# Performance work log

Hardware: AMD Instinct MI355X
Metric: run time of the kernel (lower is better)

The kernel has to match this reference:

```python
import jax, jax.numpy as jnp
import numpy as np
import math

B, S, H, NH = 2, 2048, 2048, 16
HD = H // NH
BASE = 10000.0


def _rope_tables():
    inv_freq = 1.0 / (BASE ** (np.arange(0, HD, 2, dtype=np.float32) / HD))
    t = np.arange(S, dtype=np.float32)
    freqs = np.einsum('i,j->ij', t, inv_freq)          # [S, HD/2]
    emb = np.concatenate([freqs, freqs], axis=-1)       # [S, HD]
    return jnp.asarray(np.cos(emb)), jnp.asarray(np.sin(emb))


def setup_inputs() -> dict:
    key = jax.random.key(0)
    ks = jax.random.split(key, 6)
    scale = 1.0 / math.sqrt(H)
    cos, sin = _rope_tables()
    causal = np.triu(np.full((S, S), -1e9, dtype=np.float32), k=1)
    attn_bias = jnp.broadcast_to(jnp.asarray(causal)[None, None], (B, 1, S, S))
    return {
        'hidden_states': jax.random.normal(ks[0], (B, S, H), jnp.float32),
        'masks': jnp.zeros((B, S, S), jnp.float32),
        'attn_bias': attn_bias,
        'cos': cos,
        'sin': sin,
        'wq': jax.random.normal(ks[1], (H, H), jnp.float32) * scale,
        'wk': jax.random.normal(ks[2], (H, H), jnp.float32) * scale,
        'wv': jax.random.normal(ks[3], (H, H), jnp.float32) * scale,
        'wo': jax.random.normal(ks[4], (H, H), jnp.float32) * scale,
        'position_ids': jnp.broadcast_to(jnp.arange(S, dtype=jnp.int64)[None], (B, S)),
    }


def _rotate_half(x):
    x1, x2 = x[..., : x.shape[-1] // 2], x[..., x.shape[-1] // 2:]
    return jnp.concatenate([-x2, x1], axis=-1)


def reference(hidden_states, masks, attn_bias, cos, sin, wq, wk, wv, wo, position_ids):
    b, s, h = hidden_states.shape
    nh, hd = NH, HD
    # QKV projections (torch Linear: x @ W.T), split heads -> [b, nh, s, hd]
    def proj(w):
        return (hidden_states @ w.T).reshape(b, s, nh, hd).transpose(0, 2, 1, 3)
    q, k, v = proj(wq), proj(wk), proj(wv)
    # RoPE
    cos_p = cos[position_ids][:, None]  # [b, 1, s, hd]
    sin_p = sin[position_ids][:, None]
    q = q * cos_p + _rotate_half(q) * sin_p
    k = k * cos_p + _rotate_half(k) * sin_p
    # attention scores with additive masks (mx_attn branch, fp math)
    att = jnp.einsum('bhqd,bhkd->bhqk', q / math.sqrt(hd), k)
    att = att + attn_bias + masks[:, None]
    att = jax.nn.softmax(att, axis=-1)
    out = jnp.einsum('bhqk,bhkd->bhqd', att, v)
    out = out.transpose(0, 2, 1, 3).reshape(b, s, h)
    return out @ wo.T
```

## Files before the change

### kernel.cpp

```cpp
#include <hip/hip_runtime.h>
#include <stdint.h>

#define B_  2
#define S_  2048
#define H_  2048
#define NH_ 16
#define HD_ 128

typedef __bf16 v8bf __attribute__((ext_vector_type(8)));
typedef float  v4f  __attribute__((ext_vector_type(4)));

__device__ __forceinline__ float b2f(unsigned short u) {
  union { unsigned int i; float f; } x; x.i = ((unsigned int)u) << 16; return x.f;
}
__device__ __forceinline__ unsigned short f2b(float f) {
  union { float f; unsigned int i; } x; x.f = f;
  unsigned int r = x.i + 0x7FFFu + ((x.i >> 16) & 1u);
  return (unsigned short)(r >> 16);
}

__device__ __forceinline__ void async16(const void* g, void* l) {
  __builtin_amdgcn_global_load_lds(
      (const __attribute__((address_space(1))) void*)g,
      (__attribute__((address_space(3))) void*)l, 16, 0, 0);
}

__global__ __launch_bounds__(256) void cvt_f32_bf16(const float* __restrict__ src,
                                                    unsigned short* __restrict__ dst,
                                                    int n4) {
  int i = blockIdx.x * 256 + threadIdx.x;
  if (i < n4) {
    float4 f = *(const float4*)(src + (size_t)i * 4);
    ushort4 u;
    u.x = f2b(f.x); u.y = f2b(f.y); u.z = f2b(f.z); u.w = f2b(f.w);
    *(ushort4*)(dst + (size_t)i * 4) = u;
  }
}

__device__ __forceinline__ void gemm_tile_nt(const unsigned short* __restrict__ A,
                                             const unsigned short* __restrict__ Bm,
                                             int m0, int n0, int Kdim,
                                             unsigned short* As, unsigned short* Bs,
                                             v4f (&acc)[4][4]) {
  const int tid = threadIdx.x;
  const int lane = tid & 63, w = tid >> 6;
  const int lr = lane & 15, lg = lane >> 4;
  const int wm = (w >> 1) * 64, wn = (w & 1) * 64;

  for (int k0 = 0; k0 < Kdim; k0 += 32) {
    __syncthreads();
#pragma unroll
    for (int i = 0; i < 2; ++i) {
      const int cbase = i * 256 + w * 64;
      const int cc = cbase + lane;
      const int row = cc >> 2, col = (cc & 3) << 3;
      async16(A  + (size_t)(m0 + row) * Kdim + k0 + col, (char*)As + (size_t)cbase * 16);
      async16(Bm + (size_t)(n0 + row) * Kdim + k0 + col, (char*)Bs + (size_t)cbase * 16);
    }
    __syncthreads();
    v8bf a[4], bb[4];
#pragma unroll
    for (int i = 0; i < 4; i++) a[i]  = *(const v8bf*)(As + (wm + i * 16 + lr) * 32 + lg * 8);
#pragma unroll
    for (int i = 0; i < 4; i++) bb[i] = *(const v8bf*)(Bs + (wn + i * 16 + lr) * 32 + lg * 8);
#pragma unroll
    for (int mi = 0; mi < 4; mi++)
#pragma unroll
      for (int ni = 0; ni < 4; ni++)
        acc[mi][ni] = __builtin_amdgcn_mfma_f32_16x16x32_bf16(a[mi], bb[ni], acc[mi][ni], 0, 0, 0);
  }
}

__global__ __launch_bounds__(256, 2) void gemm_qkv(const unsigned short* __restrict__ X,
                                                   const unsigned short* __restrict__ Wq,
                                                   const unsigned short* __restrict__ Wk,
                                                   const unsigned short* __restrict__ Wv,
                                                   unsigned short* __restrict__ Qo,
                                                   unsigned short* __restrict__ Ko,
                                                   unsigned short* __restrict__ Vo) {
  __shared__ unsigned short As[128 * 32], Bs[128 * 32];
  const int m0 = blockIdx.x * 128;
  const int ny = blockIdx.y;
  const int sel = ny >> 4;
  const unsigned short* Bm = (sel == 0) ? Wq : (sel == 1 ? Wk : Wv);
  unsigned short* Out = (sel == 0) ? Qo : (sel == 1 ? Ko : Vo);
  const int n0 = (ny & 15) * 128;

  v4f acc[4][4];
#pragma unroll
  for (int i = 0; i < 4; i++)
#pragma unroll
    for (int j = 0; j < 4; j++) { v4f z = {0.f, 0.f, 0.f, 0.f}; acc[i][j] = z; }

  gemm_tile_nt(X, Bm, m0, n0, H_, As, Bs, acc);

  const int lane = threadIdx.x & 63, w = threadIdx.x >> 6;
  const int lr = lane & 15, lg = lane >> 4;
  const int wm = (w >> 1) * 64, wn = (w & 1) * 64;
#pragma unroll
  for (int mi = 0; mi < 4; mi++)
#pragma unroll
    for (int ni = 0; ni < 4; ni++)
#pragma unroll
      for (int r = 0; r < 4; r++)
        Out[(size_t)(m0 + wm + mi * 16 + lg * 4 + r) * H_ + n0 + wn + ni * 16 + lr] =
            f2b(acc[mi][ni][r]);
}

__global__ __launch_bounds__(256, 2) void gemm_out(const unsigned short* __restrict__ A,
                                                   const unsigned short* __restrict__ Wo,
                                                   float* __restrict__ Out) {
  __shared__ unsigned short As[128 * 32], Bs[128 * 32];
  const int m0 = blockIdx.x * 128;
  const int n0 = blockIdx.y * 128;

  v4f acc[4][4];
#pragma unroll
  for (int i = 0; i < 4; i++)
#pragma unroll
    for (int j = 0; j < 4; j++) { v4f z = {0.f, 0.f, 0.f, 0.f}; acc[i][j] = z; }

  gemm_tile_nt(A, Wo, m0, n0, H_, As, Bs, acc);

  const int lane = threadIdx.x & 63, w = threadIdx.x >> 6;
  const int lr = lane & 15, lg = lane >> 4;
  const int wm = (w >> 1) * 64, wn = (w & 1) * 64;
#pragma unroll
  for (int mi = 0; mi < 4; mi++)
#pragma unroll
    for (int ni = 0; ni < 4; ni++)
#pragma unroll
      for (int r = 0; r < 4; r++)
        Out[(size_t)(m0 + wm + mi * 16 + lg * 4 + r) * H_ + n0 + wn + ni * 16 + lr] =
            acc[mi][ni][r];
}

__global__ __launch_bounds__(256) void rope_kernel(unsigned short* __restrict__ Q,
                                                   unsigned short* __restrict__ K,
                                                   const float* __restrict__ cosT,
                                                   const float* __restrict__ sinT) {
  unsigned idx = blockIdx.x * 256 + threadIdx.x;
  int dq = (idx & 15) * 4;
  int h  = (idx >> 4) & 15;
  int s  = (idx >> 8) & 2047;
  int b  = idx >> 19;
  size_t base = ((size_t)(b * S_ + s)) * H_ + h * HD_;
  const float* cr = cosT + (size_t)s * HD_;
  const float* sr = sinT + (size_t)s * HD_;
  float c1[4], c2[4], s1[4], s2[4];
#pragma unroll
  for (int j = 0; j < 4; j++) {
    c1[j] = cr[dq + j]; c2[j] = cr[64 + dq + j];
    s1[j] = sr[dq + j]; s2[j] = sr[64 + dq + j];
  }
#pragma unroll
  for (int a = 0; a < 2; a++) {
    unsigned short* P = a == 0 ? Q : K;
    const float sc = (a == 0) ? 0.088388347648318447f : 1.0f;
    ushort4 u1 = *(ushort4*)(P + base + dq);
    ushort4 u2 = *(ushort4*)(P + base + 64 + dq);
    float x1[4] = {b2f(u1.x), b2f(u1.y), b2f(u1.z), b2f(u1.w)};
    float x2[4] = {b2f(u2.x), b2f(u2.y), b2f(u2.z), b2f(u2.w)};
    ushort4 o1, o2;
    o1.x = f2b((x1[0] * c1[0] - x2[0] * s1[0]) * sc);
    o1.y = f2b((x1[1] * c1[1] - x2[1] * s1[1]) * sc);
    o1.z = f2b((x1[2] * c1[2] - x2[2] * s1[2]) * sc);
    o1.w = f2b((x1[3] * c1[3] - x2[3] * s1[3]) * sc);
    o2.x = f2b((x2[0] * c2[0] + x1[0] * s2[0]) * sc);
    o2.y = f2b((x2[1] * c2[1] + x1[1] * s2[1]) * sc);
    o2.z = f2b((x2[2] * c2[2] + x1[2] * s2[2]) * sc);
    o2.w = f2b((x2[3] * c2[3] + x1[3] * s2[3]) * sc);
    *(ushort4*)(P + base + dq) = o1;
    *(ushort4*)(P + base + 64 + dq) = o2;
  }
}

__global__ __launch_bounds__(256) void transpose_v(const unsigned short* __restrict__ Vb,
                                                   unsigned short* __restrict__ Vt) {
  __shared__ unsigned short tile[64][130];
  const int tid = threadIdx.x;
  const int s0 = blockIdx.x * 64;
  const int h = blockIdx.y, b = blockIdx.z;
  for (int i = tid; i < 64 * 64; i += 256) {
    int s = i >> 6, dp = i & 63;
    *(ushort2*)&tile[s][dp * 2] =
        *(const ushort2*)(Vb + (size_t)(b * S_ + s0 + s) * H_ + h * HD_ + dp * 2);
  }
  __syncthreads();
  for (int i = tid; i < 128 * 64; i += 256) {
    int d = i >> 6, s = i & 63;
    Vt[((size_t)((b * NH_ + h) * HD_) + d) * S_ + s0 + s] = tile[s][d];
  }
}

#define KT_ 64

__global__ __launch_bounds__(256, 2) void attn_kernel(const unsigned short* __restrict__ Qb,
                                                      const unsigned short* __restrict__ Kb,
                                                      const unsigned short* __restrict__ Vt,
                                                      unsigned short* __restrict__ Ob) {
  __shared__ __align__(16) char smem[54272];
  unsigned short* Ks = (unsigned short*)smem;
  unsigned short* Vs = (unsigned short*)(smem + 17408);
  unsigned short* Ps = (unsigned short*)(smem + 35840);

  const int tid = threadIdx.x, lane = tid & 63, w = tid >> 6;
  const int lr = lane & 15, lg = lane >> 4;
  const int qt = blockIdx.x, h = blockIdx.y, b = blockIdx.z;
  const int q0 = qt * 128;
  const int wrow = q0 + w * 32;

  v8bf qf[2][4];
#pragma unroll
  for (int mt = 0; mt < 2; mt++)
#pragma unroll
    for (int ks = 0; ks < 4; ks++)
      qf[mt][ks] = *(const v8bf*)(Qb + (size_t)(b * S_ + wrow + mt * 16 + lr) * H_ +
                                  h * HD_ + ks * 32 + lg * 8);

  v4f o[2][8];
#pragma unroll
  for (int mt = 0; mt < 2; mt++)
#pragma unroll
    for (int nt = 0; nt < 8; nt++) { v4f z = {0.f, 0.f, 0.f, 0.f}; o[mt][nt] = z; }
  float mst[2][4], lst[2][4];
#pragma unroll
  for (int mt = 0; mt < 2; mt++)
#pragma unroll
    for (int r = 0; r < 4; r++) { mst[mt][r] = -1e30f; lst[mt][r] = 0.f; }

  const int nkt = (q0 + 128) / KT_;
  for (int kt = 0; kt < nkt; kt++) {
    const int k0 = kt * KT_;
    __syncthreads();
    for (int i = 0; i < 5; ++i) {
      int cbase = i * 256 + w * 64;
      if (cbase < 1088) {
        int cc = cbase + lane;
        int row = cc / 17, pos = cc % 17;
        int p2 = (pos == 16) ? 0 : pos;
        async16(Kb + (size_t)(b * S_ + k0 + row) * H_ + h * HD_ + p2 * 8,
                (char*)Ks + (size_t)cbase * 16);
      }
    }
    for (int i = 0; i < 5; ++i) {
      int cbase = i * 256 + w * 64;
      if (cbase < 1152) {
        int cc = cbase + lane;
        int row = cc / 9, pos = cc % 9;
        int p2 = (pos == 8) ? 0 : pos;
        async16(Vt + ((size_t)((b * NH_ + h) * HD_ + row)) * S_ + k0 + p2 * 8,
                (char*)Vs + (size_t)cbase * 16);
      }
    }
    __syncthreads();

    if (k0 <= wrow + 31) {
      v4f sacc[2][4];
#pragma unroll
      for (int mt = 0; mt < 2; mt++)
#pragma unroll
        for (int nt = 0; nt < 4; nt++) { v4f z = {0.f, 0.f, 0.f, 0.f}; sacc[mt][nt] = z; }
#pragma unroll
      for (int nt = 0; nt < 4; nt++) {
        v8bf kf[4];
#pragma unroll
        for (int ks = 0; ks < 4; ks++)
          kf[ks] = *(const v8bf*)(Ks + (nt * 16 + lr) * 136 + ks * 32 + lg * 8);
#pragma unroll
        for (int mt = 0; mt < 2; mt++)
#pragma unroll
          for (int ks = 0; ks < 4; ks++)
            sacc[mt][nt] =
                __builtin_amdgcn_mfma_f32_16x16x32_bf16(qf[mt][ks], kf[ks], sacc[mt][nt], 0, 0, 0);
      }
      if (k0 + KT_ - 1 > wrow) {
#pragma unroll
        for (int mt = 0; mt < 2; mt++)
#pragma unroll
          for (int nt = 0; nt < 4; nt++)
#pragma unroll
            for (int r = 0; r < 4; r++) {
              int key = k0 + nt * 16 + lr;
              int query = wrow + mt * 16 + lg * 4 + r;
              if (key > query) sacc[mt][nt][r] = -1e30f;
            }
      }
#pragma unroll
      for (int mt = 0; mt < 2; mt++) {
        float rmax[4], alpha[4], rsum[4];
#pragma unroll
        for (int r = 0; r < 4; r++) {
          float v = fmaxf(fmaxf(sacc[mt][0][r], sacc[mt][1][r]),
                          fmaxf(sacc[mt][2][r], sacc[mt][3][r]));
#pragma unroll
          for (int off = 8; off >= 1; off >>= 1) v = fmaxf(v, __shfl_xor(v, off, 64));
          rmax[r] = v;
        }
#pragma unroll
        for (int r = 0; r < 4; r++) {
          float mnew = fmaxf(mst[mt][r], rmax[r]);
          alpha[r] = __expf(mst[mt][r] - mnew);
          mst[mt][r] = mnew;
          rsum[r] = 0.f;
        }
#pragma unroll
        for (int nt = 0; nt < 4; nt++)
#pragma unroll
          for (int r = 0; r < 4; r++) {
            float p = __expf(sacc[mt][nt][r] - mst[mt][r]);
            rsum[r] += p;
            Ps[w * 2304 + (mt * 16 + lg * 4 + r) * 72 + nt * 16 + lr] = f2b(p);
          }
#pragma unroll
        for (int r = 0; r < 4; r++) {
#pragma unroll
          for (int off = 8; off >= 1; off >>= 1) rsum[r] += __shfl_xor(rsum[r], off, 64);
          lst[mt][r] = lst[mt][r] * alpha[r] + rsum[r];
        }
#pragma unroll
        for (int nt = 0; nt < 8; nt++)
#pragma unroll
          for (int r = 0; r < 4; r++) o[mt][nt][r] *= alpha[r];
      }
      asm volatile("" ::: "memory");
      v8bf af[2][2];
#pragma unroll
      for (int mt = 0; mt < 2; mt++)
#pragma unroll
        for (int ks = 0; ks < 2; ks++)
          af[mt][ks] = *(const v8bf*)(Ps + w * 2304 + (mt * 16 + lr) * 72 + ks * 32 + lg * 8);
#pragma unroll
      for (int nt = 0; nt < 8; nt++) {
        v8bf bv[2];
#pragma unroll
        for (int ks = 0; ks < 2; ks++)
          bv[ks] = *(const v8bf*)(Vs + (nt * 16 + lr) * 72 + ks * 32 + lg * 8);
#pragma unroll
        for (int mt = 0; mt < 2; mt++)
#pragma unroll
          for (int ks = 0; ks < 2; ks++)
            o[mt][nt] = __builtin_amdgcn_mfma_f32_16x16x32_bf16(af[mt][ks], bv[ks], o[mt][nt], 0, 0, 0);
      }
    }
  }
#pragma unroll
  for (int mt = 0; mt < 2; mt++) {
    float inv[4];
#pragma unroll
    for (int r = 0; r < 4; r++) inv[r] = 1.f / lst[mt][r];
#pragma unroll
    for (int nt = 0; nt < 8; nt++)
#pragma unroll
      for (int r = 0; r < 4; r++) {
        int row = wrow + mt * 16 + lg * 4 + r;
        int col = h * HD_ + nt * 16 + lr;
        Ob[(size_t)(b * S_ + row) * H_ + col] = f2b(o[mt][nt][r] * inv[r]);
      }
  }
}

extern "C" void kernel_launch(void* const* d_in, const int* in_sizes, int n_in,
                              void* d_out, int out_size, void* d_ws, size_t ws_size,
                              hipStream_t stream) {
  const float* hidden = (const float*)d_in[0];
  const float* cosT = (const float*)d_in[3];
  const float* sinT = (const float*)d_in[4];
  const float* wq = (const float*)d_in[5];
  const float* wk = (const float*)d_in[6];
  const float* wv = (const float*)d_in[7];
  const float* wo = (const float*)d_in[8];
  float* out = (float*)d_out;

  char* p = (char*)d_ws;
  const size_t SZ_X = (size_t)4096 * 2048 * 2;
  const size_t SZ_W = (size_t)2048 * 2048 * 2;
  unsigned short* Xb  = (unsigned short*)p; p += SZ_X;
  unsigned short* Wqb = (unsigned short*)p; p += SZ_W;
  unsigned short* Wkb = (unsigned short*)p; p += SZ_W;
  unsigned short* Wvb = (unsigned short*)p; p += SZ_W;
  unsigned short* Wob = (unsigned short*)p; p += SZ_W;
  unsigned short* Qb  = (unsigned short*)p; p += SZ_X;
  unsigned short* Kb  = (unsigned short*)p; p += SZ_X;
  unsigned short* Vb  = (unsigned short*)p; p += SZ_X;
  unsigned short* Vt  = (unsigned short*)p; p += SZ_X;
  unsigned short* Ob  = Vb;

  cvt_f32_bf16<<<8192, 256, 0, stream>>>(hidden, Xb, 2097152);
  cvt_f32_bf16<<<4096, 256, 0, stream>>>(wq, Wqb, 1048576);
  cvt_f32_bf16<<<4096, 256, 0, stream>>>(wk, Wkb, 1048576);
  cvt_f32_bf16<<<4096, 256, 0, stream>>>(wv, Wvb, 1048576);
  cvt_f32_bf16<<<4096, 256, 0, stream>>>(wo, Wob, 1048576);

  gemm_qkv<<<dim3(32, 48), 256, 0, stream>>>(Xb, Wqb, Wkb, Wvb, Qb, Kb, Vb);
  rope_kernel<<<4096, 256, 0, stream>>>(Qb, Kb, cosT, sinT);
  transpose_v<<<dim3(32, 16, 2), 256, 0, stream>>>(Vb, Vt);
  attn_kernel<<<dim3(16, 16, 2), 256, 0, stream>>>(Qb, Kb, Vt, Ob);
  gemm_out<<<dim3(32, 16), 256, 0, stream>>>(Ob, Wob, out);
}
```

Before: 490.7 us.

## Pair causal query tiles per block with 8 waves and exp2 softmax

```diff
diff --git a/kernel.cpp b/kernel.cpp
--- a/kernel.cpp
+++ b/kernel.cpp
@@ -156,7 +156,7 @@
 #pragma unroll
   for (int a = 0; a < 2; a++) {
     unsigned short* P = a == 0 ? Q : K;
-    const float sc = (a == 0) ? 0.088388347648318447f : 1.0f;
+    const float sc = (a == 0) ? (float)(0.08838834764831845 * 1.4426950408889634) : 1.0f;
     ushort4 u1 = *(ushort4*)(P + base + dq);
     ushort4 u2 = *(ushort4*)(P + base + 64 + dq);
     float x1[4] = {b2f(u1.x), b2f(u1.y), b2f(u1.z), b2f(u1.w)};
@@ -195,7 +195,7 @@
 
 #define KT_ 64
 
-__global__ __launch_bounds__(256, 2) void attn_kernel(const unsigned short* __restrict__ Qb,
+__global__ __launch_bounds__(512, 2) void attn_kernel(const unsigned short* __restrict__ Qb,
                                                       const unsigned short* __restrict__ Kb,
                                                       const unsigned short* __restrict__ Vt,
                                                       unsigned short* __restrict__ Ob) {
@@ -206,157 +206,143 @@
 
   const int tid = threadIdx.x, lane = tid & 63, w = tid >> 6;
   const int lr = lane & 15, lg = lane >> 4;
-  const int qt = blockIdx.x, h = blockIdx.y, b = blockIdx.z;
-  const int q0 = qt * 128;
-  const int wrow = q0 + w * 32;
-
-  v8bf qf[2][4];
-#pragma unroll
-  for (int mt = 0; mt < 2; mt++)
+  const int qp = blockIdx.x, h = blockIdx.y, b = blockIdx.z;
+
+#pragma unroll 1
+  for (int pass = 0; pass < 2; pass++) {
+    const int qt = pass ? (15 - qp) : qp;
+    const int q0 = qt * 128;
+    const int wrow = q0 + w * 16;
+
+    v8bf qf[4];
 #pragma unroll
     for (int ks = 0; ks < 4; ks++)
-      qf[mt][ks] = *(const v8bf*)(Qb + (size_t)(b * S_ + wrow + mt * 16 + lr) * H_ +
-                                  h * HD_ + ks * 32 + lg * 8);
-
-  v4f o[2][8];
-#pragma unroll
-  for (int mt = 0; mt < 2; mt++)
-#pragma unroll
-    for (int nt = 0; nt < 8; nt++) { v4f z = {0.f, 0.f, 0.f, 0.f}; o[mt][nt] = z; }
-  float mst[2][4], lst[2][4];
-#pragma unroll
-  for (int mt = 0; mt < 2; mt++)
-#pragma unroll
-    for (int r = 0; r < 4; r++) { mst[mt][r] = -1e30f; lst[mt][r] = 0.f; }
-
-  const int nkt = (q0 + 128) / KT_;
-  for (int kt = 0; kt < nkt; kt++) {
-    const int k0 = kt * KT_;
-    __syncthreads();
-    for (int i = 0; i < 5; ++i) {
-      int cbase = i * 256 + w * 64;
-      if (cbase < 1088) {
-        int cc = cbase + lane;
-        int row = cc / 17, pos = cc % 17;
-        int p2 = (pos == 16) ? 0 : pos;
-        async16(Kb + (size_t)(b * S_ + k0 + row) * H_ + h * HD_ + p2 * 8,
-                (char*)Ks + (size_t)cbase * 16);
+      qf[ks] = *(const v8bf*)(Qb + (size_t)(b * S_ + wrow + lr) * H_ +
+                              h * HD_ + ks * 32 + lg * 8);
+
+    v4f o[8];
+#pragma unroll
+    for (int nt = 0; nt < 8; nt++) { v4f z = {0.f, 0.f, 0.f, 0.f}; o[nt] = z; }
+    float mst[4], lst[4];
+#pragma unroll
+    for (int r = 0; r < 4; r++) { mst[r] = -1e30f; lst[r] = 0.f; }
+
+    const int nkt = (q0 + 128) / KT_;
+    for (int kt = 0; kt < nkt; kt++) {
+      const int k0 = kt * KT_;
+      __syncthreads();
+#pragma unroll
+      for (int i = 0; i < 3; ++i) {
+        int cbase = i * 512 + w * 64;
+        if (cbase < 1088) {
+          int cc = cbase + lane;
+          int row = cc / 17, pos = cc % 17;
+          int p2 = (pos == 16) ? 0 : pos;
+          async16(Kb + (size_t)(b * S_ + k0 + row) * H_ + h * HD_ + p2 * 8,
+                  (char*)Ks + (size_t)cbase * 16);
+        }
+      }
+#pragma unroll
+      for (int i = 0; i < 3; ++i) {
+        int cbase = i * 512 + w * 64;
+        if (cbase < 1152) {
+          int cc = cbase + lane;
+          int row = cc / 9, pos = cc % 9;
+          int p2 = (pos == 8) ? 0 : pos;
+          async16(Vt + ((size_t)((b * NH_ + h) * HD_ + row)) * S_ + k0 + p2 * 8,
+                  (char*)Vs + (size_t)cbase * 16);
+        }
+      }
+      __syncthreads();
+
+      if (k0 <= wrow + 15) {
+        v4f sacc[4];
+#pragma unroll
+        for (int nt = 0; nt < 4; nt++) { v4f z = {0.f, 0.f, 0.f, 0.f}; sacc[nt] = z; }
+#pragma unroll
+        for (int nt = 0; nt < 4; nt++) {
+          v8bf kf[4];
+#pragma unroll
+          for (int ks = 0; ks < 4; ks++)
+            kf[ks] = *(const v8bf*)(Ks + (nt * 16 + lr) * 136 + ks * 32 + lg * 8);
+#pragma unroll
+          for (int ks = 0; ks < 4; ks++)
+            sacc[nt] =
+                __builtin_amdgcn_mfma_f32_16x16x32_bf16(qf[ks], kf[ks], sacc[nt], 0, 0, 0);
+        }
+        if (k0 + KT_ - 1 > wrow) {
+#pragma unroll
+          for (int nt = 0; nt < 4; nt++)
+#pragma unroll
+            for (int r = 0; r < 4; r++) {
+              int key = k0 + nt * 16 + lr;
+              int query = wrow + lg * 4 + r;
+              if (key > query) sacc[nt][r] = -1e30f;
+            }
+        }
+        float rmax[4], alpha[4], rsum[4];
+#pragma unroll
+        for (int r = 0; r < 4; r++) {
+          float v = fmaxf(fmaxf(sacc[0][r], sacc[1][r]),
+                          fmaxf(sacc[2][r], sacc[3][r]));
+#pragma unroll
+          for (int off = 8; off >= 1; off >>= 1) v = fmaxf(v, __shfl_xor(v, off, 64));
+          rmax[r] = v;
+        }
+#pragma unroll
+        for (int r = 0; r < 4; r++) {
+          float mnew = fmaxf(mst[r], rmax[r]);
+          alpha[r] = exp2f(mst[r] - mnew);
+          mst[r] = mnew;
+          rsum[r] = 0.f;
+        }
+#pragma unroll
+        for (int nt = 0; nt < 4; nt++)
+#pragma unroll
+          for (int r = 0; r < 4; r++) {
+            float p = exp2f(sacc[nt][r] - mst[r]);
+            rsum[r] += p;
+            Ps[w * 1152 + (lg * 4 + r) * 72 + nt * 16 + lr] = f2b(p);
+          }
+#pragma unroll
+        for (int r = 0; r < 4; r++) {
+#pragma unroll
+          for (int off = 8; off >= 1; off >>= 1) rsum[r] += __shfl_xor(rsum[r], off, 64);
+          lst[r] = lst[r] * alpha[r] + rsum[r];
+        }
+#pragma unroll
+        for (int nt = 0; nt < 8; nt++)
+#pragma unroll
+          for (int r = 0; r < 4; r++) o[nt][r] *= alpha[r];
+        asm volatile("" ::: "memory");
+        v8bf af[2];
+#pragma unroll
+        for (int ks = 0; ks < 2; ks++)
+          af[ks] = *(const v8bf*)(Ps + w * 1152 + lr * 72 + ks * 32 + lg * 8);
+#pragma unroll
+        for (int nt = 0; nt < 8; nt++) {
+          v8bf bv[2];
+#pragma unroll
+          for (int ks = 0; ks < 2; ks++)
+            bv[ks] = *(const v8bf*)(Vs + (nt * 16 + lr) * 72 + ks * 32 + lg * 8);
+#pragma unroll
+          for (int ks = 0; ks < 2; ks++)
+            o[nt] = __builtin_amdgcn_mfma_f32_16x16x32_bf16(af[ks], bv[ks], o[nt], 0, 0, 0);
+        }
       }
     }
-    for (int i = 0; i < 5; ++i) {
-      int cbase = i * 256 + w * 64;
-      if (cbase < 1152) {
-        int cc = cbase + lane;
-        int row = cc / 9, pos = cc % 9;
-        int p2 = (pos == 8) ? 0 : pos;
-        async16(Vt + ((size_t)((b * NH_ + h) * HD_ + row)) * S_ + k0 + p2 * 8,
-                (char*)Vs + (size_t)cbase * 16);
+    float inv[4];
+#pragma unroll
+    for (int r = 0; r < 4; r++) inv[r] = 1.f / lst[r];
+#pragma unroll
+    for (int nt = 0; nt < 8; nt++)
+#pragma unroll
+      for (int r = 0; r < 4; r++) {
+        int row = wrow + lg * 4 + r;
+        int col = h * HD_ + nt * 16 + lr;
+        Ob[(size_t)(b * S_ + row) * H_ + col] = f2b(o[nt][r] * inv[r]);
       }
-    }
     __syncthreads();
-
-    if (k0 <= wrow + 31) {
-      v4f sacc[2][4];
-#pragma unroll
-      for (int mt = 0; mt < 2; mt++)
-#pragma unroll
-        for (int nt = 0; nt < 4; nt++) { v4f z = {0.f, 0.f, 0.f, 0.f}; sacc[mt][nt] = z; }
-#pragma unroll
-      for (int nt = 0; nt < 4; nt++) {
-        v8bf kf[4];
-#pragma unroll
-        for (int ks = 0; ks < 4; ks++)
-          kf[ks] = *(const v8bf*)(Ks + (nt * 16 + lr) * 136 + ks * 32 + lg * 8);
-#pragma unroll
-        for (int mt = 0; mt < 2; mt++)
-#pragma unroll
-          for (int ks = 0; ks < 4; ks++)
-            sacc[mt][nt] =
-                __builtin_amdgcn_mfma_f32_16x16x32_bf16(qf[mt][ks], kf[ks], sacc[mt][nt], 0, 0, 0);
-      }
-      if (k0 + KT_ - 1 > wrow) {
-#pragma unroll
-        for (int mt = 0; mt < 2; mt++)
-#pragma unroll
-          for (int nt = 0; nt < 4; nt++)
-#pragma unroll
-            for (int r = 0; r < 4; r++) {
-              int key = k0 + nt * 16 + lr;
-              int query = wrow + mt * 16 + lg * 4 + r;
-              if (key > query) sacc[mt][nt][r] = -1e30f;
-            }
-      }
-#pragma unroll
-      for (int mt = 0; mt < 2; mt++) {
-        float rmax[4], alpha[4], rsum[4];
-#pragma unroll
-        for (int r = 0; r < 4; r++) {
-          float v = fmaxf(fmaxf(sacc[mt][0][r], sacc[mt][1][r]),
-                          fmaxf(sacc[mt][2][r], sacc[mt][3][r]));
-#pragma unroll
-          for (int off = 8; off >= 1; off >>= 1) v = fmaxf(v, __shfl_xor(v, off, 64));
-          rmax[r] = v;
-        }
-#pragma unroll
-        for (int r = 0; r < 4; r++) {
-          float mnew = fmaxf(mst[mt][r], rmax[r]);
-          alpha[r] = __expf(mst[mt][r] - mnew);
-          mst[mt][r] = mnew;
-          rsum[r] = 0.f;
-        }
-#pragma unroll
-        for (int nt = 0; nt < 4; nt++)
-#pragma unroll
-          for (int r = 0; r < 4; r++) {
-            float p = __expf(sacc[mt][nt][r] - mst[mt][r]);
-            rsum[r] += p;
-            Ps[w * 2304 + (mt * 16 + lg * 4 + r) * 72 + nt * 16 + lr] = f2b(p);
-          }
-#pragma unroll
-        for (int r = 0; r < 4; r++) {
-#pragma unroll
-          for (int off = 8; off >= 1; off >>= 1) rsum[r] += __shfl_xor(rsum[r], off, 64);
-          lst[mt][r] = lst[mt][r] * alpha[r] + rsum[r];
-        }
-#pragma unroll
-        for (int nt = 0; nt < 8; nt++)
-#pragma unroll
-          for (int r = 0; r < 4; r++) o[mt][nt][r] *= alpha[r];
-      }
-      asm volatile("" ::: "memory");
-      v8bf af[2][2];
-#pragma unroll
-      for (int mt = 0; mt < 2; mt++)
-#pragma unroll
-        for (int ks = 0; ks < 2; ks++)
-          af[mt][ks] = *(const v8bf*)(Ps + w * 2304 + (mt * 16 + lr) * 72 + ks * 32 + lg * 8);
-#pragma unroll
-      for (int nt = 0; nt < 8; nt++) {
-        v8bf bv[2];
-#pragma unroll
-        for (int ks = 0; ks < 2; ks++)
-          bv[ks] = *(const v8bf*)(Vs + (nt * 16 + lr) * 72 + ks * 32 + lg * 8);
-#pragma unroll
-        for (int mt = 0; mt < 2; mt++)
-#pragma unroll
-          for (int ks = 0; ks < 2; ks++)
-            o[mt][nt] = __builtin_amdgcn_mfma_f32_16x16x32_bf16(af[mt][ks], bv[ks], o[mt][nt], 0, 0, 0);
-      }
-    }
-  }
-#pragma unroll
-  for (int mt = 0; mt < 2; mt++) {
-    float inv[4];
-#pragma unroll
-    for (int r = 0; r < 4; r++) inv[r] = 1.f / lst[mt][r];
-#pragma unroll
-    for (int nt = 0; nt < 8; nt++)
-#pragma unroll
-      for (int r = 0; r < 4; r++) {
-        int row = wrow + mt * 16 + lg * 4 + r;
-        int col = h * HD_ + nt * 16 + lr;
-        Ob[(size_t)(b * S_ + row) * H_ + col] = f2b(o[mt][nt][r] * inv[r]);
-      }
   }
 }
 
@@ -395,6 +381,6 @@
   gemm_qkv<<<dim3(32, 48), 256, 0, stream>>>(Xb, Wqb, Wkb, Wvb, Qb, Kb, Vb);
   rope_kernel<<<4096, 256, 0, stream>>>(Qb, Kb, cosT, sinT);
   transpose_v<<<dim3(32, 16, 2), 256, 0, stream>>>(Vb, Vt);
-  attn_kernel<<<dim3(16, 16, 2), 256, 0, stream>>>(Qb, Kb, Vt, Ob);
+  attn_kernel<<<dim3(8, 16, 2), 512, 0, stream>>>(Qb, Kb, Vt, Ob);
   gemm_out<<<dim3(32, 16), 256, 0, stream>>>(Ob, Wob, out);
 }
```

New measurement: 470.4 us. -4.1%, faster.
